# Performance work log

Measured on AMD Instinct MI355X. Metric: run time of the kernel, lower is better.

Reference implementation:

```python
import jax, jax.numpy as jnp
import numpy as np

H_SIZE = 1024
N_HEADS = 16
D_K = H_SIZE // N_HEADS


def setup_inputs() -> dict:
    key = jax.random.key(0)
    ks = jax.random.split(key, 12)
    s = 1.0 / np.sqrt(H_SIZE)
    inp = {
        "x": jax.random.normal(ks[0], (2, 2048, H_SIZE), dtype=jnp.float32),
        "Wq": jax.random.uniform(ks[1], (H_SIZE, H_SIZE), minval=-s, maxval=s),
        "bq": jax.random.uniform(ks[2], (H_SIZE,), minval=-s, maxval=s),
        "Wk": jax.random.uniform(ks[3], (H_SIZE, H_SIZE), minval=-s, maxval=s),
        "bk": jax.random.uniform(ks[4], (H_SIZE,), minval=-s, maxval=s),
        "Wv": jax.random.uniform(ks[5], (H_SIZE, H_SIZE), minval=-s, maxval=s),
        "bv": jax.random.uniform(ks[6], (H_SIZE,), minval=-s, maxval=s),
        "Wo": jax.random.uniform(ks[7], (H_SIZE, H_SIZE), minval=-s, maxval=s),
        "bo": jax.random.uniform(ks[8], (H_SIZE,), minval=-s, maxval=s),
        "ln_gamma": jnp.ones((H_SIZE,), dtype=jnp.float32),
        "ln_beta": jnp.zeros((H_SIZE,), dtype=jnp.float32),
    }
    return inp


def reference(x, Wq, bq, Wk, bk, Wv, bv, Wo, bo, ln_gamma, ln_beta):
    B, L, H = x.shape
    residual = x
    # QKV projections -> [B, n_heads, L, d_k]
    def proj(W, b):
        return (x @ W.T + b).reshape(B, L, N_HEADS, D_K).transpose(0, 2, 1, 3)
    q = proj(Wq, bq)
    k = proj(Wk, bk)
    v = proj(Wv, bv)
    # scaled dot-product attention (dropout = identity in eval mode)
    scores = jnp.einsum("bhqd,bhkd->bhqk", q, k) / jnp.sqrt(jnp.float32(D_K))
    attn = jax.nn.softmax(scores, axis=-1)
    out = jnp.einsum("bhqk,bhkd->bhqd", attn, v)
    out = out.transpose(0, 2, 1, 3).reshape(B, L, H)
    out = out @ Wo.T + bo
    # residual + LayerNorm
    y = out + residual
    mu = jnp.mean(y, axis=-1, keepdims=True)
    var = jnp.var(y, axis=-1, keepdims=True)
    y = (y - mu) / jnp.sqrt(var + 1e-5) * ln_gamma + ln_beta
    return y
```

## Files before the change

kernel.cpp:

```cpp
#include <hip/hip_runtime.h>

#define H_SIZE 1024
#define N_HEADS 16
#define D_K 64
#define SEQ 2048
#define BATCH 2
#define M_TOT 4096

typedef __bf16 __attribute__((ext_vector_type(8))) bf16_8;
typedef float __attribute__((ext_vector_type(4))) f32x4;
typedef float __attribute__((ext_vector_type(16))) f32x16;
typedef int __attribute__((ext_vector_type(4))) int4v;

#define SWZ(r) ((((r) & 7) ^ (((r) >> 3) & 7)))

__device__ __forceinline__ ushort f2bf(float f) {
    unsigned int u = __float_as_uint(f);
    unsigned int r = (u + 0x7FFFu + ((u >> 16) & 1u)) >> 16;
    return (ushort)r;
}

__device__ __forceinline__ unsigned int cvtpk(float lo, float hi) {
    unsigned int r;
    asm("v_cvt_pk_bf16_f32 %0, %1, %2" : "=v"(r) : "v"(lo), "v"(hi));
    return r;
}

__device__ __forceinline__ float exp2_raw(float x) {
    float r;
    asm("v_exp_f32 %0, %1" : "=v"(r) : "v"(x));
    return r;
}

__device__ __forceinline__ void gld16(void* lds, const void* g) {
    __builtin_amdgcn_global_load_lds(
        (const __attribute__((address_space(1))) unsigned int*)g,
        (__attribute__((address_space(3))) unsigned int*)lds, 16, 0, 0);
}

__global__ __launch_bounds__(256) void cast_all_kernel(
    const float* __restrict__ x, const float* __restrict__ wq, const float* __restrict__ wk,
    const float* __restrict__ wv, const float* __restrict__ wo,
    ushort* __restrict__ xb, ushort* __restrict__ wqb, ushort* __restrict__ wkb,
    ushort* __restrict__ wvb, ushort* __restrict__ wob) {
    int i = blockIdx.x * 256 + threadIdx.x;
    const float* src;
    ushort* dst;
    int off;
    if (i < 1048576) {
        src = x; dst = xb; off = i;
    } else {
        int j = i - 1048576;
        int w = j >> 18;
        off = j & 262143;
        src = (w == 0) ? wq : (w == 1) ? wk : (w == 2) ? wv : wo;
        dst = (w == 0) ? wqb : (w == 1) ? wkb : (w == 2) ? wvb : wob;
    }
    float4 v = ((const float4*)src)[off];
    ushort4 o;
    o.x = f2bf(v.x); o.y = f2bf(v.y); o.z = f2bf(v.z); o.w = f2bf(v.w);
    ((ushort4*)dst)[off] = o;
}

__global__ __launch_bounds__(256) void gemm_qkv(
    const ushort* __restrict__ A, const ushort* __restrict__ wq,
    const ushort* __restrict__ wk, const ushort* __restrict__ wv,
    const float* __restrict__ bq, const float* __restrict__ bk, const float* __restrict__ bv,
    ushort* __restrict__ Qb, ushort* __restrict__ Kb, ushort* __restrict__ Vtb) {
    constexpr int BK = 32;
    __shared__ ushort As[3][128 * BK];
    __shared__ ushort Bs[3][128 * BK];
    const int tid = threadIdx.x;
    const int lane = tid & 63, wid = tid >> 6;
    const int wr = wid >> 1, wc = wid & 1;
    const int hi = lane >> 4, lo = lane & 15;
    const int bm0 = blockIdx.x * 128;
    const int t3 = blockIdx.y >> 3;
    const int bn0 = (blockIdx.y & 7) * 128;
    const ushort* Bw = (t3 == 0) ? wq : (t3 == 1) ? wk : wv;
    const float* bias = (t3 == 0) ? bq : (t3 == 1) ? bk : bv;

    f32x4 acc[4][4] = {};

    const int srow = tid >> 2;
    const int sseg = ((tid & 3) ^ ((tid >> 3) & 3)) * 8;
    const ushort* gaB = A + (size_t)(bm0 + srow) * H_SIZE + sseg;
    const ushort* gbB = Bw + (size_t)(bn0 + srow) * H_SIZE + sseg;
    const int ldsOff = tid * 16;

#define STAGE(ba, bb, kt)                                 \
    {                                                     \
        char* la = (char*)(ba) + ldsOff;                  \
        char* lb = (char*)(bb) + ldsOff;                  \
        gld16(la, gaB + (kt));                            \
        gld16(la + 4096, gaB + 64 * H_SIZE + (kt));       \
        gld16(lb, gbB + (kt));                            \
        gld16(lb + 4096, gbB + 64 * H_SIZE + (kt));       \
    }

    STAGE(&As[0][0], &Bs[0][0], 0);
    STAGE(&As[1][0], &Bs[1][0], BK);
    asm volatile("s_waitcnt vmcnt(4)" ::: "memory");
    __builtin_amdgcn_s_barrier();
    __builtin_amdgcn_sched_barrier(0);

    constexpr int NT = H_SIZE / BK;
    const int rxv = (lo >> 1) & 3;
    int cur = 0;
    for (int t = 0; t < NT; t++) {
        int c2 = cur + 2; if (c2 >= 3) c2 -= 3;
        if (t + 2 < NT) STAGE(&As[c2][0], &Bs[c2][0], (t + 2) * BK);
        {
            bf16_8 af[4], bfv[4];
            const ushort* pa = &As[cur][(wr * 64 + lo) * BK + ((hi ^ rxv) * 8)];
            const ushort* pb = &Bs[cur][(wc * 64 + lo) * BK + ((hi ^ rxv) * 8)];
#pragma unroll
            for (int i = 0; i < 4; i++) af[i] = *(const bf16_8*)(pa + i * 16 * BK);
#pragma unroll
            for (int i = 0; i < 4; i++) bfv[i] = *(const bf16_8*)(pb + i * 16 * BK);
#pragma unroll
            for (int mi = 0; mi < 4; mi++)
#pragma unroll
                for (int ni = 0; ni < 4; ni++)
                    acc[mi][ni] = __builtin_amdgcn_mfma_f32_16x16x32_bf16(
                        af[mi], bfv[ni], acc[mi][ni], 0, 0, 0);
        }
        if (t + 1 < NT) {
            if (t + 2 < NT) { asm volatile("s_waitcnt vmcnt(4)" ::: "memory"); }
            else            { asm volatile("s_waitcnt vmcnt(0)" ::: "memory"); }
            __builtin_amdgcn_s_barrier();
            __builtin_amdgcn_sched_barrier(0);
        }
        cur = cur + 1; if (cur >= 3) cur -= 3;
    }
#undef STAGE

#pragma unroll
    for (int mi = 0; mi < 4; mi++) {
#pragma unroll
        for (int ni = 0; ni < 4; ni++) {
            const int row0 = bm0 + wr * 64 + mi * 16 + hi * 4;
            const int col = bn0 + wc * 64 + ni * 16 + lo;
            const float bv = bias[col];
            const int h = col >> 6, dk = col & 63;
            if (t3 == 2) {
                const int b = row0 >> 11, l0 = row0 & 2047;
                const int lsw0 = (l0 & ~63) | (((((l0 >> 3) & 7) ^ SWZ(dk)) & 7) << 3) | (l0 & 7);
                uint2 o;
                o.x = cvtpk(acc[mi][ni][0] + bv, acc[mi][ni][1] + bv);
                o.y = cvtpk(acc[mi][ni][2] + bv, acc[mi][ni][3] + bv);
                *(uint2*)&Vtb[((size_t)(b * N_HEADS + h) * D_K + dk) * SEQ + lsw0] = o;
            } else {
#pragma unroll
                for (int rr = 0; rr < 4; rr++) {
                    const int m = row0 + rr;
                    const int b = m >> 11, l = m & 2047;
                    float val = acc[mi][ni][rr] + bv;
                    if (t3 == 0) {
                        Qb[((size_t)(b * N_HEADS + h) * SEQ + l) * D_K + dk] =
                            f2bf(val * 0.18033688f);
                    } else {
                        int dks = ((((dk >> 3) ^ SWZ(l & 63)) & 7) << 3) | (dk & 7);
                        Kb[((size_t)(b * N_HEADS + h) * SEQ + l) * D_K + dks] = f2bf(val);
                    }
                }
            }
        }
    }
}

__global__ __launch_bounds__(256) void gemm_o(const ushort* __restrict__ A,
                                              const ushort* __restrict__ Bw,
                                              const float* __restrict__ bias,
                                              const float* __restrict__ resid,
                                              float* __restrict__ outp) {
    constexpr int BK = 32;
    __shared__ ushort As[3][128 * BK];
    __shared__ ushort Bs[3][64 * BK];
    const int tid = threadIdx.x;
    const int lane = tid & 63, wid = tid >> 6;
    const int wr = wid >> 1, wc = wid & 1;
    const int hi = lane >> 4, lo = lane & 15;
    const int bm0 = blockIdx.x * 128, bn0 = blockIdx.y * 64;

    f32x4 acc[4][2] = {};

    const int srow = tid >> 2;
    const int sseg = ((tid & 3) ^ ((tid >> 3) & 3)) * 8;
    const ushort* gaB = A + (size_t)(bm0 + srow) * H_SIZE + sseg;
    const ushort* gbB = Bw + (size_t)(bn0 + srow) * H_SIZE + sseg;
    const int ldsOff = tid * 16;

#define STAGE(ba, bb, kt)                                 \
    {                                                     \
        char* la = (char*)(ba) + ldsOff;                  \
        gld16(la, gaB + (kt));                            \
        gld16(la + 4096, gaB + 64 * H_SIZE + (kt));       \
        gld16((char*)(bb) + ldsOff, gbB + (kt));          \
    }

    STAGE(&As[0][0], &Bs[0][0], 0);
    STAGE(&As[1][0], &Bs[1][0], BK);
    asm volatile("s_waitcnt vmcnt(3)" ::: "memory");
    __builtin_amdgcn_s_barrier();
    __builtin_amdgcn_sched_barrier(0);

    constexpr int NT = H_SIZE / BK;
    const int rxv = (lo >> 1) & 3;
    int cur = 0;
    for (int t = 0; t < NT; t++) {
        int c2 = cur + 2; if (c2 >= 3) c2 -= 3;
        if (t + 2 < NT) STAGE(&As[c2][0], &Bs[c2][0], (t + 2) * BK);
        {
            bf16_8 af[4], bfv[2];
            const ushort* pa = &As[cur][(wr * 64 + lo) * BK + ((hi ^ rxv) * 8)];
            const ushort* pb = &Bs[cur][(wc * 32 + lo) * BK + ((hi ^ rxv) * 8)];
#pragma unroll
            for (int i = 0; i < 4; i++) af[i] = *(const bf16_8*)(pa + i * 16 * BK);
#pragma unroll
            for (int i = 0; i < 2; i++) bfv[i] = *(const bf16_8*)(pb + i * 16 * BK);
#pragma unroll
            for (int mi = 0; mi < 4; mi++)
#pragma unroll
                for (int ni = 0; ni < 2; ni++)
                    acc[mi][ni] = __builtin_amdgcn_mfma_f32_16x16x32_bf16(
                        af[mi], bfv[ni], acc[mi][ni], 0, 0, 0);
        }
        if (t + 1 < NT) {
            if (t + 2 < NT) { asm volatile("s_waitcnt vmcnt(3)" ::: "memory"); }
            else            { asm volatile("s_waitcnt vmcnt(0)" ::: "memory"); }
            __builtin_amdgcn_s_barrier();
            __builtin_amdgcn_sched_barrier(0);
        }
        cur = cur + 1; if (cur >= 3) cur -= 3;
    }
#undef STAGE

#pragma unroll
    for (int mi = 0; mi < 4; mi++) {
#pragma unroll
        for (int ni = 0; ni < 2; ni++) {
            const int row0 = bm0 + wr * 64 + mi * 16 + hi * 4;
            const int col = bn0 + wc * 32 + ni * 16 + lo;
            const float bv = bias[col];
#pragma unroll
            for (int rr = 0; rr < 4; rr++) {
                const int m = row0 + rr;
                outp[(size_t)m * H_SIZE + col] =
                    acc[mi][ni][rr] + bv + resid[(size_t)m * H_SIZE + col];
            }
        }
    }
}

__global__ __launch_bounds__(256) void attn_kernel(const ushort* __restrict__ Q,
                                                   const ushort* __restrict__ Ksw,
                                                   const ushort* __restrict__ Vsw,
                                                   ushort* __restrict__ Out) {
    __shared__ ushort Ks[3][64 * 64];
    __shared__ ushort Vs[3][64 * 64];
    __shared__ float lsum_lds[4][32];
    const int lane = threadIdx.x & 63, wid = threadIdx.x >> 6;
    const int h32 = lane >> 5, q32 = lane & 31;

    const int lin = blockIdx.y * gridDim.x + blockIdx.x;
    const int nlin = (lin & 7) * 64 + (lin >> 3);
    const int bx = nlin & 15;
    const int bh = nlin >> 4;
    const int q0 = bx * 128 + wid * 32;
    const ushort* Qh = Q + (size_t)bh * SEQ * D_K;
    const ushort* Kp = Ksw + (size_t)bh * SEQ * D_K;
    const ushort* Vp = Vsw + (size_t)bh * D_K * SEQ;

    bf16_8 qf[4];
#pragma unroll
    for (int tt = 0; tt < 4; tt++)
        qf[tt] = *(const bf16_8*)(Qh + (size_t)(q0 + q32) * D_K + tt * 16 + h32 * 8);

    f32x16 oacc0 = {}, oacc1 = {};
    float ls = 0.f;

    const int koff = wid * 2048 + lane * 16;
    const int vrow = wid * 16 + (lane >> 3);
    const int vseg = (lane & 7) * 16;

#define STAGE(bb, kt)                                                             \
    {                                                                             \
        const char* kg = (const char*)(Kp + (size_t)(kt) * D_K);                  \
        char* kl = (char*)&Ks[bb][0];                                             \
        gld16(kl + koff, kg + koff);                                              \
        gld16(kl + koff + 1024, kg + koff + 1024);                                \
        char* vl = (char*)&Vs[bb][0];                                             \
        gld16(vl + vrow * 128 + vseg,                                             \
              (const char*)(Vp + (size_t)vrow * SEQ + (kt)) + vseg);              \
        gld16(vl + (vrow + 8) * 128 + vseg,                                       \
              (const char*)(Vp + (size_t)(vrow + 8) * SEQ + (kt)) + vseg);        \
    }

    STAGE(0, 0);
    STAGE(1, 64);
    asm volatile("s_waitcnt vmcnt(4)" ::: "memory");
    __builtin_amdgcn_s_barrier();
    __builtin_amdgcn_sched_barrier(0);

    constexpr int NTT = SEQ / 64;
    int cur = 0;
    for (int t = 0; t < NTT; t++) {
        int c2 = cur + 2; if (c2 >= 3) c2 -= 3;
        if (t + 2 < NTT) STAGE(c2, (t + 2) * 64);
        const ushort* kb = &Ks[cur][0];
        const ushort* vb = &Vs[cur][0];

        f32x16 st0 = {}, st1 = {};
        __builtin_amdgcn_s_setprio(1);
#pragma unroll
        for (int tt = 0; tt < 4; tt++) {
            const int krow = q32;
            int sg = (2 * tt + h32) ^ SWZ(krow);
            bf16_8 kf = *(const bf16_8*)(kb + krow * 64 + sg * 8);
            st0 = __builtin_amdgcn_mfma_f32_32x32x16_bf16(kf, qf[tt], st0, 0, 0, 0);
        }
#pragma unroll
        for (int tt = 0; tt < 4; tt++) {
            const int krow = 32 + q32;
            int sg = (2 * tt + h32) ^ SWZ(krow);
            bf16_8 kf = *(const bf16_8*)(kb + krow * 64 + sg * 8);
            st1 = __builtin_amdgcn_mfma_f32_32x32x16_bf16(kf, qf[tt], st1, 0, 0, 0);
        }
        __builtin_amdgcn_s_setprio(0);

        union { unsigned int w[4]; bf16_8 v; } pf00, pf01;
        float part0 = 0.f;
#pragma unroll
        for (int rr = 0; rr < 16; rr++) { st0[rr] = exp2_raw(st0[rr]); part0 += st0[rr]; }
#pragma unroll
        for (int i = 0; i < 2; i++) {
            unsigned int a = cvtpk(st0[2 * i], st0[2 * i + 1]);
            unsigned int b = cvtpk(st0[4 + 2 * i], st0[4 + 2 * i + 1]);
            asm volatile("v_permlane32_swap_b32 %0, %1" : "+v"(a), "+v"(b));
            pf00.w[i] = a; pf00.w[2 + i] = b;
            unsigned int c = cvtpk(st0[8 + 2 * i], st0[8 + 2 * i + 1]);
            unsigned int d = cvtpk(st0[12 + 2 * i], st0[12 + 2 * i + 1]);
            asm volatile("v_permlane32_swap_b32 %0, %1" : "+v"(c), "+v"(d));
            pf01.w[i] = c; pf01.w[2 + i] = d;
        }
        ls += part0 + __shfl_xor(part0, 32);

        __builtin_amdgcn_s_setprio(1);
        {
            const int vr0 = q32;
            int sg0 = (h32) ^ SWZ(vr0);
            int sg1 = (2 + h32) ^ SWZ(vr0);
            bf16_8 vf0 = *(const bf16_8*)(vb + vr0 * 64 + sg0 * 8);
            bf16_8 vf1 = *(const bf16_8*)(vb + vr0 * 64 + sg1 * 8);
            oacc0 = __builtin_amdgcn_mfma_f32_32x32x16_bf16(pf00.v, vf0, oacc0, 0, 0, 0);
            oacc0 = __builtin_amdgcn_mfma_f32_32x32x16_bf16(pf01.v, vf1, oacc0, 0, 0, 0);
            const int vr1 = 32 + q32;
            int sg2 = (h32) ^ SWZ(vr1);
            int sg3 = (2 + h32) ^ SWZ(vr1);
            bf16_8 vf2 = *(const bf16_8*)(vb + vr1 * 64 + sg2 * 8);
            bf16_8 vf3 = *(const bf16_8*)(vb + vr1 * 64 + sg3 * 8);
            oacc1 = __builtin_amdgcn_mfma_f32_32x32x16_bf16(pf00.v, vf2, oacc1, 0, 0, 0);
            oacc1 = __builtin_amdgcn_mfma_f32_32x32x16_bf16(pf01.v, vf3, oacc1, 0, 0, 0);
        }
        __builtin_amdgcn_s_setprio(0);

        union { unsigned int w[4]; bf16_8 v; } pf10, pf11;
        float part1 = 0.f;
#pragma unroll
        for (int rr = 0; rr < 16; rr++) { st1[rr] = exp2_raw(st1[rr]); part1 += st1[rr]; }
#pragma unroll
        for (int i = 0; i < 2; i++) {
            unsigned int a = cvtpk(st1[2 * i], st1[2 * i + 1]);
            unsigned int b = cvtpk(st1[4 + 2 * i], st1[4 + 2 * i + 1]);
            asm volatile("v_permlane32_swap_b32 %0, %1" : "+v"(a), "+v"(b));
            pf10.w[i] = a; pf10.w[2 + i] = b;
            unsigned int c = cvtpk(st1[8 + 2 * i], st1[8 + 2 * i + 1]);
            unsigned int d = cvtpk(st1[12 + 2 * i], st1[12 + 2 * i + 1]);
            asm volatile("v_permlane32_swap_b32 %0, %1" : "+v"(c), "+v"(d));
            pf11.w[i] = c; pf11.w[2 + i] = d;
        }
        ls += part1 + __shfl_xor(part1, 32);

        __builtin_amdgcn_s_setprio(1);
        {
            const int vr0 = q32;
            int sg0 = (4 + h32) ^ SWZ(vr0);
            int sg1 = (6 + h32) ^ SWZ(vr0);
            bf16_8 vf0 = *(const bf16_8*)(vb + vr0 * 64 + sg0 * 8);
            bf16_8 vf1 = *(const bf16_8*)(vb + vr0 * 64 + sg1 * 8);
            oacc0 = __builtin_amdgcn_mfma_f32_32x32x16_bf16(pf10.v, vf0, oacc0, 0, 0, 0);
            oacc0 = __builtin_amdgcn_mfma_f32_32x32x16_bf16(pf11.v, vf1, oacc0, 0, 0, 0);
            const int vr1 = 32 + q32;
            int sg2 = (4 + h32) ^ SWZ(vr1);
            int sg3 = (6 + h32) ^ SWZ(vr1);
            bf16_8 vf2 = *(const bf16_8*)(vb + vr1 * 64 + sg2 * 8);
            bf16_8 vf3 = *(const bf16_8*)(vb + vr1 * 64 + sg3 * 8);
            oacc1 = __builtin_amdgcn_mfma_f32_32x32x16_bf16(pf10.v, vf2, oacc1, 0, 0, 0);
            oacc1 = __builtin_amdgcn_mfma_f32_32x32x16_bf16(pf11.v, vf3, oacc1, 0, 0, 0);
        }
        __builtin_amdgcn_s_setprio(0);

        if (t + 1 < NTT) {
            if (t + 2 < NTT) { asm volatile("s_waitcnt vmcnt(4)" ::: "memory"); }
            else             { asm volatile("s_waitcnt vmcnt(0)" ::: "memory"); }
            __builtin_amdgcn_s_barrier();
            __builtin_amdgcn_sched_barrier(0);
        }
        cur = cur + 1; if (cur >= 3) cur -= 3;
    }
#undef STAGE

    if (lane < 32) lsum_lds[wid][q32] = 1.0f / ls;
    const int b = bh >> 4, h = bh & 15;
#pragma unroll
    for (int rr = 0; rr < 16; rr++) {
        const int qloc = (rr & 3) + 8 * (rr >> 2) + 4 * h32;
        const float inv = lsum_lds[wid][qloc];
        const int l = q0 + qloc;
        ushort* orow = Out + ((size_t)(b * SEQ + l)) * H_SIZE + h * 64;
        orow[q32] = f2bf(oacc0[rr] * inv);
        orow[32 + q32] = f2bf(oacc1[rr] * inv);
    }
}

__global__ __launch_bounds__(256) void ln_kernel(float* __restrict__ y,
                                                 const float* __restrict__ gamma,
                                                 const float* __restrict__ beta) {
    const int row = blockIdx.x;
    float4* p = (float4*)(y + (size_t)row * H_SIZE);
    float4 v = p[threadIdx.x];
    float s = v.x + v.y + v.z + v.w;
    float s2 = v.x * v.x + v.y * v.y + v.z * v.z + v.w * v.w;
#pragma unroll
    for (int off = 1; off < 64; off <<= 1) {
        s += __shfl_xor(s, off);
        s2 += __shfl_xor(s2, off);
    }
    __shared__ float ss[4], ss2[4];
    const int wid = threadIdx.x >> 6, lane = threadIdx.x & 63;
    if (lane == 0) { ss[wid] = s; ss2[wid] = s2; }
    __syncthreads();
    s = ss[0] + ss[1] + ss[2] + ss[3];
    s2 = ss2[0] + ss2[1] + ss2[2] + ss2[3];
    const float mean = s * (1.0f / H_SIZE);
    const float var = s2 * (1.0f / H_SIZE) - mean * mean;
    const float rstd = rsqrtf(var + 1e-5f);
    const float4 g = ((const float4*)gamma)[threadIdx.x];
    const float4 bt = ((const float4*)beta)[threadIdx.x];
    float4 o;
    o.x = (v.x - mean) * rstd * g.x + bt.x;
    o.y = (v.y - mean) * rstd * g.y + bt.y;
    o.z = (v.z - mean) * rstd * g.z + bt.z;
    o.w = (v.w - mean) * rstd * g.w + bt.w;
    p[threadIdx.x] = o;
}

extern "C" void kernel_launch(void* const* d_in, const int* in_sizes, int n_in,
                              void* d_out, int out_size, void* d_ws, size_t ws_size,
                              hipStream_t stream) {
    const float* x = (const float*)d_in[0];
    const float* Wq = (const float*)d_in[1];
    const float* bq = (const float*)d_in[2];
    const float* Wk = (const float*)d_in[3];
    const float* bk = (const float*)d_in[4];
    const float* Wv = (const float*)d_in[5];
    const float* bv = (const float*)d_in[6];
    const float* Wo = (const float*)d_in[7];
    const float* bo = (const float*)d_in[8];
    const float* gamma = (const float*)d_in[9];
    const float* beta = (const float*)d_in[10];

    char* ws = (char*)d_ws;
    ushort* xb  = (ushort*)(ws);
    ushort* wqb = (ushort*)(ws + (8u << 20));
    ushort* wkb = (ushort*)(ws + (10u << 20));
    ushort* wvb = (ushort*)(ws + (12u << 20));
    ushort* wob = (ushort*)(ws + (14u << 20));
    ushort* Qb  = (ushort*)(ws + (16u << 20));
    ushort* Kb  = (ushort*)(ws + (24u << 20));
    ushort* Vtb = (ushort*)(ws + (32u << 20));
    ushort* Ao  = (ushort*)(ws + (40u << 20));

    cast_all_kernel<<<8192, 256, 0, stream>>>(x, Wq, Wk, Wv, Wo, xb, wqb, wkb, wvb, wob);

    dim3 gq(M_TOT / 128, 24);
    gemm_qkv<<<gq, 256, 0, stream>>>(xb, wqb, wkb, wvb, bq, bk, bv, Qb, Kb, Vtb);

    dim3 g2(SEQ / 128, BATCH * N_HEADS);
    attn_kernel<<<g2, 256, 0, stream>>>(Qb, Kb, Vtb, Ao);

    dim3 go(M_TOT / 128, H_SIZE / 64);
    gemm_o<<<go, 256, 0, stream>>>(Ao, wob, bo, x, (float*)d_out);

    ln_kernel<<<M_TOT, 256, 0, stream>>>((float*)d_out, gamma, beta);
}
```

Before: 136.3 us.

## Fuse fp32-to-bf16 casts into GEMM loaders and drop standalone cast kernel

Removes the separate cast kernel and has the QKV and output-projection GEMMs read fp32 x and weights directly, converting to bf16 in registers before writing to LDS. The pipeline changes from triple-buffered async global-to-LDS loads to register-staged double buffering with __syncthreads. This saves one launch and a full fp32 read plus bf16 write/read round trip. In exchange, each GEMM block reads twice the bytes per tile and re-converts data that other blocks share, and it loses the direct-to-LDS async loads.

```diff
diff --git a/kernel.cpp b/kernel.cpp
--- a/kernel.cpp
+++ b/kernel.cpp
@@ -38,38 +38,14 @@
         (__attribute__((address_space(3))) unsigned int*)lds, 16, 0, 0);
 }
 
-__global__ __launch_bounds__(256) void cast_all_kernel(
-    const float* __restrict__ x, const float* __restrict__ wq, const float* __restrict__ wk,
-    const float* __restrict__ wv, const float* __restrict__ wo,
-    ushort* __restrict__ xb, ushort* __restrict__ wqb, ushort* __restrict__ wkb,
-    ushort* __restrict__ wvb, ushort* __restrict__ wob) {
-    int i = blockIdx.x * 256 + threadIdx.x;
-    const float* src;
-    ushort* dst;
-    int off;
-    if (i < 1048576) {
-        src = x; dst = xb; off = i;
-    } else {
-        int j = i - 1048576;
-        int w = j >> 18;
-        off = j & 262143;
-        src = (w == 0) ? wq : (w == 1) ? wk : (w == 2) ? wv : wo;
-        dst = (w == 0) ? wqb : (w == 1) ? wkb : (w == 2) ? wvb : wob;
-    }
-    float4 v = ((const float4*)src)[off];
-    ushort4 o;
-    o.x = f2bf(v.x); o.y = f2bf(v.y); o.z = f2bf(v.z); o.w = f2bf(v.w);
-    ((ushort4*)dst)[off] = o;
-}
-
 __global__ __launch_bounds__(256) void gemm_qkv(
-    const ushort* __restrict__ A, const ushort* __restrict__ wq,
-    const ushort* __restrict__ wk, const ushort* __restrict__ wv,
+    const float* __restrict__ X, const float* __restrict__ Wqf,
+    const float* __restrict__ Wkf, const float* __restrict__ Wvf,
     const float* __restrict__ bq, const float* __restrict__ bk, const float* __restrict__ bv,
     ushort* __restrict__ Qb, ushort* __restrict__ Kb, ushort* __restrict__ Vtb) {
     constexpr int BK = 32;
-    __shared__ ushort As[3][128 * BK];
-    __shared__ ushort Bs[3][128 * BK];
+    __shared__ ushort As[2][128 * BK];
+    __shared__ ushort Bs[2][128 * BK];
     const int tid = threadIdx.x;
     const int lane = tid & 63, wid = tid >> 6;
     const int wr = wid >> 1, wc = wid & 1;
@@ -77,39 +53,58 @@
     const int bm0 = blockIdx.x * 128;
     const int t3 = blockIdx.y >> 3;
     const int bn0 = (blockIdx.y & 7) * 128;
-    const ushort* Bw = (t3 == 0) ? wq : (t3 == 1) ? wk : wv;
+    const float* Bw = (t3 == 0) ? Wqf : (t3 == 1) ? Wkf : Wvf;
     const float* bias = (t3 == 0) ? bq : (t3 == 1) ? bk : bv;
 
     f32x4 acc[4][4] = {};
 
     const int srow = tid >> 2;
-    const int sseg = ((tid & 3) ^ ((tid >> 3) & 3)) * 8;
-    const ushort* gaB = A + (size_t)(bm0 + srow) * H_SIZE + sseg;
-    const ushort* gbB = Bw + (size_t)(bn0 + srow) * H_SIZE + sseg;
-    const int ldsOff = tid * 16;
-
-#define STAGE(ba, bb, kt)                                 \
-    {                                                     \
-        char* la = (char*)(ba) + ldsOff;                  \
-        char* lb = (char*)(bb) + ldsOff;                  \
-        gld16(la, gaB + (kt));                            \
-        gld16(la + 4096, gaB + 64 * H_SIZE + (kt));       \
-        gld16(lb, gbB + (kt));                            \
-        gld16(lb + 4096, gbB + 64 * H_SIZE + (kt));       \
-    }
-
-    STAGE(&As[0][0], &Bs[0][0], 0);
-    STAGE(&As[1][0], &Bs[1][0], BK);
-    asm volatile("s_waitcnt vmcnt(4)" ::: "memory");
-    __builtin_amdgcn_s_barrier();
-    __builtin_amdgcn_sched_barrier(0);
+    const int c4 = tid & 3;
+    const int pseg = (c4 ^ ((srow >> 1) & 3)) * 8;
+    const float* gA0 = X + (size_t)(bm0 + srow) * H_SIZE + c4 * 8;
+    const float* gA1 = gA0 + 64 * H_SIZE;
+    const float* gB0 = Bw + (size_t)(bn0 + srow) * H_SIZE + c4 * 8;
+    const float* gB1 = gB0 + 64 * H_SIZE;
+
+    float4 ra0, ra1, ra2, ra3, rb0, rb1, rb2, rb3;
+
+#define LOADREG(kt)                                        \
+    {                                                      \
+        ra0 = *(const float4*)(gA0 + (kt));                \
+        ra1 = *(const float4*)(gA0 + (kt) + 4);            \
+        ra2 = *(const float4*)(gA1 + (kt));                \
+        ra3 = *(const float4*)(gA1 + (kt) + 4);            \
+        rb0 = *(const float4*)(gB0 + (kt));                \
+        rb1 = *(const float4*)(gB0 + (kt) + 4);            \
+        rb2 = *(const float4*)(gB1 + (kt));                \
+        rb3 = *(const float4*)(gB1 + (kt) + 4);            \
+    }
+#define CVTWRITE(bb)                                                           \
+    {                                                                          \
+        uint4 w;                                                               \
+        w.x = cvtpk(ra0.x, ra0.y); w.y = cvtpk(ra0.z, ra0.w);                  \
+        w.z = cvtpk(ra1.x, ra1.y); w.w = cvtpk(ra1.z, ra1.w);                  \
+        *(uint4*)&As[bb][srow * BK + pseg] = w;                                \
+        w.x = cvtpk(ra2.x, ra2.y); w.y = cvtpk(ra2.z, ra2.w);                  \
+        w.z = cvtpk(ra3.x, ra3.y); w.w = cvtpk(ra3.z, ra3.w);                  \
+        *(uint4*)&As[bb][(srow + 64) * BK + pseg] = w;                         \
+        w.x = cvtpk(rb0.x, rb0.y); w.y = cvtpk(rb0.z, rb0.w);                  \
+        w.z = cvtpk(rb1.x, rb1.y); w.w = cvtpk(rb1.z, rb1.w);                  \
+        *(uint4*)&Bs[bb][srow * BK + pseg] = w;                                \
+        w.x = cvtpk(rb2.x, rb2.y); w.y = cvtpk(rb2.z, rb2.w);                  \
+        w.z = cvtpk(rb3.x, rb3.y); w.w = cvtpk(rb3.z, rb3.w);                  \
+        *(uint4*)&Bs[bb][(srow + 64) * BK + pseg] = w;                         \
+    }
+
+    LOADREG(0);
+    CVTWRITE(0);
+    __syncthreads();
 
     constexpr int NT = H_SIZE / BK;
     const int rxv = (lo >> 1) & 3;
-    int cur = 0;
     for (int t = 0; t < NT; t++) {
-        int c2 = cur + 2; if (c2 >= 3) c2 -= 3;
-        if (t + 2 < NT) STAGE(&As[c2][0], &Bs[c2][0], (t + 2) * BK);
+        const int cur = t & 1;
+        if (t + 1 < NT) LOADREG((t + 1) * BK);
         {
             bf16_8 af[4], bfv[4];
             const ushort* pa = &As[cur][(wr * 64 + lo) * BK + ((hi ^ rxv) * 8)];
@@ -126,14 +121,12 @@
                         af[mi], bfv[ni], acc[mi][ni], 0, 0, 0);
         }
         if (t + 1 < NT) {
-            if (t + 2 < NT) { asm volatile("s_waitcnt vmcnt(4)" ::: "memory"); }
-            else            { asm volatile("s_waitcnt vmcnt(0)" ::: "memory"); }
-            __builtin_amdgcn_s_barrier();
-            __builtin_amdgcn_sched_barrier(0);
-        }
-        cur = cur + 1; if (cur >= 3) cur -= 3;
-    }
-#undef STAGE
+            CVTWRITE(cur ^ 1);
+            __syncthreads();
+        }
+    }
+#undef LOADREG
+#undef CVTWRITE
 
 #pragma unroll
     for (int mi = 0; mi < 4; mi++) {
@@ -170,13 +163,13 @@
 }
 
 __global__ __launch_bounds__(256) void gemm_o(const ushort* __restrict__ A,
-                                              const ushort* __restrict__ Bw,
+                                              const float* __restrict__ Wof,
                                               const float* __restrict__ bias,
                                               const float* __restrict__ resid,
                                               float* __restrict__ outp) {
     constexpr int BK = 32;
-    __shared__ ushort As[3][128 * BK];
-    __shared__ ushort Bs[3][64 * BK];
+    __shared__ ushort As[2][128 * BK];
+    __shared__ ushort Bs[2][64 * BK];
     const int tid = threadIdx.x;
     const int lane = tid & 63, wid = tid >> 6;
     const int wr = wid >> 1, wc = wid & 1;
@@ -186,31 +179,41 @@
     f32x4 acc[4][2] = {};
 
     const int srow = tid >> 2;
-    const int sseg = ((tid & 3) ^ ((tid >> 3) & 3)) * 8;
-    const ushort* gaB = A + (size_t)(bm0 + srow) * H_SIZE + sseg;
-    const ushort* gbB = Bw + (size_t)(bn0 + srow) * H_SIZE + sseg;
-    const int ldsOff = tid * 16;
-
-#define STAGE(ba, bb, kt)                                 \
-    {                                                     \
-        char* la = (char*)(ba) + ldsOff;                  \
-        gld16(la, gaB + (kt));                            \
-        gld16(la + 4096, gaB + 64 * H_SIZE + (kt));       \
-        gld16((char*)(bb) + ldsOff, gbB + (kt));          \
-    }
-
-    STAGE(&As[0][0], &Bs[0][0], 0);
-    STAGE(&As[1][0], &Bs[1][0], BK);
-    asm volatile("s_waitcnt vmcnt(3)" ::: "memory");
-    __builtin_amdgcn_s_barrier();
-    __builtin_amdgcn_sched_barrier(0);
+    const int c4 = tid & 3;
+    const int pseg = (c4 ^ ((srow >> 1) & 3)) * 8;
+    const ushort* gA0 = A + (size_t)(bm0 + srow) * H_SIZE + c4 * 8;
+    const ushort* gA1 = gA0 + 64 * H_SIZE;
+    const float* gB0 = Wof + (size_t)(bn0 + srow) * H_SIZE + c4 * 8;
+
+    uint4 wa0, wa1;
+    float4 rb0, rb1;
+
+#define LOADREG(kt)                                        \
+    {                                                      \
+        wa0 = *(const uint4*)(gA0 + (kt));                 \
+        wa1 = *(const uint4*)(gA1 + (kt));                 \
+        rb0 = *(const float4*)(gB0 + (kt));                \
+        rb1 = *(const float4*)(gB0 + (kt) + 4);            \
+    }
+#define CVTWRITE(bb)                                                           \
+    {                                                                          \
+        *(uint4*)&As[bb][srow * BK + pseg] = wa0;                              \
+        *(uint4*)&As[bb][(srow + 64) * BK + pseg] = wa1;                       \
+        uint4 w;                                                               \
+        w.x = cvtpk(rb0.x, rb0.y); w.y = cvtpk(rb0.z, rb0.w);                  \
+        w.z = cvtpk(rb1.x, rb1.y); w.w = cvtpk(rb1.z, rb1.w);                  \
+        *(uint4*)&Bs[bb][srow * BK + pseg] = w;                                \
+    }
+
+    LOADREG(0);
+    CVTWRITE(0);
+    __syncthreads();
 
     constexpr int NT = H_SIZE / BK;
     const int rxv = (lo >> 1) & 3;
-    int cur = 0;
     for (int t = 0; t < NT; t++) {
-        int c2 = cur + 2; if (c2 >= 3) c2 -= 3;
-        if (t + 2 < NT) STAGE(&As[c2][0], &Bs[c2][0], (t + 2) * BK);
+        const int cur = t & 1;
+        if (t + 1 < NT) LOADREG((t + 1) * BK);
         {
             bf16_8 af[4], bfv[2];
             const ushort* pa = &As[cur][(wr * 64 + lo) * BK + ((hi ^ rxv) * 8)];
@@ -227,14 +230,12 @@
                         af[mi], bfv[ni], acc[mi][ni], 0, 0, 0);
         }
         if (t + 1 < NT) {
-            if (t + 2 < NT) { asm volatile("s_waitcnt vmcnt(3)" ::: "memory"); }
-            else            { asm volatile("s_waitcnt vmcnt(0)" ::: "memory"); }
-            __builtin_amdgcn_s_barrier();
-            __builtin_amdgcn_sched_barrier(0);
-        }
-        cur = cur + 1; if (cur >= 3) cur -= 3;
-    }
-#undef STAGE
+            CVTWRITE(cur ^ 1);
+            __syncthreads();
+        }
+    }
+#undef LOADREG
+#undef CVTWRITE
 
 #pragma unroll
     for (int mi = 0; mi < 4; mi++) {
@@ -472,26 +473,19 @@
     const float* beta = (const float*)d_in[10];
 
     char* ws = (char*)d_ws;
-    ushort* xb  = (ushort*)(ws);
-    ushort* wqb = (ushort*)(ws + (8u << 20));
-    ushort* wkb = (ushort*)(ws + (10u << 20));
-    ushort* wvb = (ushort*)(ws + (12u << 20));
-    ushort* wob = (ushort*)(ws + (14u << 20));
     ushort* Qb  = (ushort*)(ws + (16u << 20));
     ushort* Kb  = (ushort*)(ws + (24u << 20));
     ushort* Vtb = (ushort*)(ws + (32u << 20));
     ushort* Ao  = (ushort*)(ws + (40u << 20));
 
-    cast_all_kernel<<<8192, 256, 0, stream>>>(x, Wq, Wk, Wv, Wo, xb, wqb, wkb, wvb, wob);
-
     dim3 gq(M_TOT / 128, 24);
-    gemm_qkv<<<gq, 256, 0, stream>>>(xb, wqb, wkb, wvb, bq, bk, bv, Qb, Kb, Vtb);
+    gemm_qkv<<<gq, 256, 0, stream>>>(x, Wq, Wk, Wv, bq, bk, bv, Qb, Kb, Vtb);
 
     dim3 g2(SEQ / 128, BATCH * N_HEADS);
     attn_kernel<<<g2, 256, 0, stream>>>(Qb, Kb, Vtb, Ao);
 
     dim3 go(M_TOT / 128, H_SIZE / 64);
-    gemm_o<<<go, 256, 0, stream>>>(Ao, wob, bo, x, (float*)d_out);
+    gemm_o<<<go, 256, 0, stream>>>(Ao, Wo, bo, x, (float*)d_out);
 
     ln_kernel<<<M_TOT, 256, 0, stream>>>((float*)d_out, gamma, beta);
 }
```

Result: faster. 132.4 us, median of 3 (-2.9%).
